# Performance work log

Hardware: AMD Instinct MI355X
Metric: run time of the kernel (lower is better)

Reference implementation:

```python
import jax, jax.numpy as jnp
import numpy as np

NEG_SLOPE = 0.2

def _spmm(row, col, val, emb, n_out):
    # sparse [n_out, n_src] @ emb[n_src, d] via gather + segment_sum
    msgs = val[:, None] * emb[col]  # [E, d]
    return jax.ops.segment_sum(msgs, row, num_segments=n_out)

def setup_inputs() -> dict:
    key = jax.random.key(0)
    ks = jax.random.split(key, 10)
    N_U, N_I, D = 100000, 200000, 64
    E_U, E_I = 1600000, 3200000
    return {
        "users_emb": jax.random.normal(ks[0], (N_U, D), dtype=jnp.float32),
        "items_emb": jax.random.normal(ks[1], (N_I, D), dtype=jnp.float32),
        "u_row": jax.random.randint(ks[2], (E_U,), 0, N_U, dtype=jnp.int32),
        "u_col": jax.random.randint(ks[3], (E_U,), 0, N_U, dtype=jnp.int32),
        "u_val": jax.random.uniform(ks[4], (E_U,), dtype=jnp.float32),
        "i_row": jax.random.randint(ks[5], (E_I,), 0, N_I, dtype=jnp.int32),
        "i_col": jax.random.randint(ks[6], (E_I,), 0, N_I, dtype=jnp.int32),
        "i_val": jax.random.uniform(ks[7], (E_I,), dtype=jnp.float32),
        "W_u": jax.random.normal(ks[8], (D, D), dtype=jnp.float32) * (6.0 / (D + D)) ** 0.5,
        "W_i": jax.random.normal(ks[9], (D, D), dtype=jnp.float32) * (6.0 / (D + D)) ** 0.5,
    }

def reference(users_emb, items_emb, u_row, u_col, u_val, i_row, i_col, i_val, W_u, W_i):
    h_u = _spmm(u_row, u_col, u_val, users_emb, users_emb.shape[0])
    h_u = jax.nn.leaky_relu(h_u @ W_u, negative_slope=NEG_SLOPE)
    h_i = _spmm(i_row, i_col, i_val, items_emb, items_emb.shape[0])
    h_i = jax.nn.leaky_relu(h_i @ W_i, negative_slope=NEG_SLOPE)
    return (h_u, h_i)
```

## Files before the change

kernel.cpp:

```cpp
#include <hip/hip_runtime.h>

#define NEG_SLOPE 0.2f

typedef unsigned int u32;

__device__ __forceinline__ unsigned short f32_to_bf16_rne(float f) {
    u32 u = __float_as_uint(f);
    u = (u + 0x7FFFu + ((u >> 16) & 1u)) >> 16;
    return (unsigned short)u;
}
__device__ __forceinline__ float bf16_to_f32(unsigned short b) {
    return __uint_as_float(((u32)b) << 16);
}

__global__ void spmm_scatter_kernel(const float* __restrict__ emb,
                                    const int* __restrict__ row,
                                    const int* __restrict__ col,
                                    const float* __restrict__ val,
                                    float* __restrict__ acc,
                                    int n_edges) {
    const int lane = threadIdx.x & 63;
    const int wpb = blockDim.x >> 6;
    const int wib = threadIdx.x >> 6;
    const int total_waves = gridDim.x * wpb;
    for (int e = blockIdx.x * wpb + wib; e < n_edges; e += total_waves) {
        const int r = row[e];
        const int c = col[e];
        const float v = val[e];
        atomicAdd(&acc[(size_t)r * 64 + lane], v * emb[(size_t)c * 64 + lane]);
    }
}

__global__ void transform_leaky_kernel(float* __restrict__ io,
                                       const float* __restrict__ W_u,
                                       const float* __restrict__ W_i,
                                       int n_u_rows, int n_total_rows) {
    __shared__ float Ws[2][64 * 64];
    for (int i = threadIdx.x; i < 64 * 64; i += blockDim.x) {
        Ws[0][i] = W_u[i];
        Ws[1][i] = W_i[i];
    }
    __syncthreads();
    const int lane = threadIdx.x & 63;
    const int wpb = blockDim.x >> 6;
    const int wib = threadIdx.x >> 6;
    const int total_waves = gridDim.x * wpb;
    for (int r = blockIdx.x * wpb + wib; r < n_total_rows; r += total_waves) {
        const float* W = (r < n_u_rows) ? Ws[0] : Ws[1];
        const float hv = io[(size_t)r * 64 + lane];
        float acc = 0.0f;
        #pragma unroll
        for (int k = 0; k < 64; ++k) {
            const float hk = __shfl(hv, k, 64);
            acc = fmaf(hk, W[k * 64 + lane], acc);
        }
        io[(size_t)r * 64 + lane] = acc > 0.0f ? acc : NEG_SLOPE * acc;
    }
}

#define PT_ROWS 64
__global__ void pretransform_both_kernel(const float* __restrict__ uemb,
                                         const float* __restrict__ iemb,
                                         const float* __restrict__ W_u,
                                         const float* __restrict__ W_i,
                                         unsigned short* __restrict__ Ybf,
                                         int n_u, int n_i, int tiles_u) {
    __shared__ float Ws[64 * 64];
    __shared__ float hs[PT_ROWS][68];

    const int tile = blockIdx.x;
    const bool is_u = tile < tiles_u;
    const float* __restrict__ emb = is_u ? uemb : iemb;
    const float* __restrict__ W = is_u ? W_u : W_i;
    const int lt = is_u ? tile : tile - tiles_u;
    const int nr = is_u ? n_u : n_i;
    const int base = lt * PT_ROWS;
    const int rows_here = min(PT_ROWS, nr - base);
    const size_t ybase = (is_u ? (size_t)base : (size_t)n_u + base) * 64;

    const int lane = threadIdx.x & 63;
    const int wid  = threadIdx.x >> 6;
    const int rsub = lane >> 4;
    const int jg   = lane & 15;

    {
        const float4* src = (const float4*)W;
        float4* dst = (float4*)Ws;
        for (int i = threadIdx.x; i < 64 * 16; i += blockDim.x) dst[i] = src[i];
    }
    for (int i = threadIdx.x; i < rows_here * 16; i += blockDim.x) {
        const int r = i >> 4, q = i & 15;
        const float4 v = ((const float4*)(emb + (size_t)(base + r) * 64))[q];
        *(float4*)&hs[r][q * 4] = v;
    }
    __syncthreads();

    #pragma unroll
    for (int quad = 0; quad < 4; ++quad) {
        const int r = (wid + quad * 4) * 4 + rsub;
        if (r < rows_here) {
            float ax = 0.f, ay = 0.f, az = 0.f, aw = 0.f;
            #pragma unroll
            for (int kq = 0; kq < 16; ++kq) {
                const float4 h = *(const float4*)&hs[r][kq * 4];
                const float4 w0 = *(const float4*)&Ws[(kq * 4 + 0) * 64 + jg * 4];
                const float4 w1 = *(const float4*)&Ws[(kq * 4 + 1) * 64 + jg * 4];
                const float4 w2 = *(const float4*)&Ws[(kq * 4 + 2) * 64 + jg * 4];
                const float4 w3 = *(const float4*)&Ws[(kq * 4 + 3) * 64 + jg * 4];
                ax = fmaf(h.x, w0.x, ax); ay = fmaf(h.x, w0.y, ay);
                az = fmaf(h.x, w0.z, az); aw = fmaf(h.x, w0.w, aw);
                ax = fmaf(h.y, w1.x, ax); ay = fmaf(h.y, w1.y, ay);
                az = fmaf(h.y, w1.z, az); aw = fmaf(h.y, w1.w, aw);
                ax = fmaf(h.z, w2.x, ax); ay = fmaf(h.z, w2.y, ay);
                az = fmaf(h.z, w2.z, az); aw = fmaf(h.z, w2.w, aw);
                ax = fmaf(h.w, w3.x, ax); ay = fmaf(h.w, w3.y, ay);
                az = fmaf(h.w, w3.z, az); aw = fmaf(h.w, w3.w, aw);
            }
            ushort4 o;
            o.x = f32_to_bf16_rne(ax);
            o.y = f32_to_bf16_rne(ay);
            o.z = f32_to_bf16_rne(az);
            o.w = f32_to_bf16_rne(aw);
            *(ushort4*)(Ybf + ybase + (size_t)r * 64 + jg * 4) = o;
        }
    }
}

__global__ void hist_fine_kernel(const int* __restrict__ rows, int n_edges,
                                 int row_off, int* __restrict__ counts, int nfb) {
    extern __shared__ int lh[];
    for (int i = threadIdx.x; i < nfb; i += blockDim.x) lh[i] = 0;
    __syncthreads();
    const int tid = blockIdx.x * blockDim.x + threadIdx.x;
    const int stride = gridDim.x * blockDim.x;
    const int n4 = n_edges >> 2;
    for (int g = tid; g < n4; g += stride) {
        const int4 r4 = ((const int4*)rows)[g];
        atomicAdd(&lh[(row_off + r4.x) >> 6], 1);
        atomicAdd(&lh[(row_off + r4.y) >> 6], 1);
        atomicAdd(&lh[(row_off + r4.z) >> 6], 1);
        atomicAdd(&lh[(row_off + r4.w) >> 6], 1);
    }
    for (int e = (n4 << 2) + tid; e < n_edges; e += stride)
        atomicAdd(&lh[(row_off + rows[e]) >> 6], 1);
    __syncthreads();
    for (int i = threadIdx.x; i < nfb; i += blockDim.x) {
        const int c = lh[i];
        if (c) atomicAdd(&counts[i], c);
    }
}

__global__ void pad_counts_kernel(const int* __restrict__ cnt,
                                  int* __restrict__ pcnt, int nfb) {
    const int i = blockIdx.x * blockDim.x + threadIdx.x;
    if (i < nfb) pcnt[i] = (cnt[i] + 7) & ~7;
}

__global__ void scan_part1_kernel(const int* __restrict__ counts, int n,
                                  int* __restrict__ partials) {
    __shared__ int s[512];
    const int gi = blockIdx.x * 512 + threadIdx.x;
    s[threadIdx.x] = (gi < n) ? counts[gi] : 0;
    __syncthreads();
    for (int off = 256; off > 0; off >>= 1) {
        if (threadIdx.x < off) s[threadIdx.x] += s[threadIdx.x + off];
        __syncthreads();
    }
    if (threadIdx.x == 0) partials[blockIdx.x] = s[0];
}

__global__ void scan_part2_kernel(int* __restrict__ partials, int nb) {
    __shared__ int s[1024];
    const int tid = threadIdx.x;
    int v = (tid < nb) ? partials[tid] : 0;
    s[tid] = v;
    __syncthreads();
    for (int off = 1; off < 1024; off <<= 1) {
        int t = (tid >= off) ? s[tid - off] : 0;
        __syncthreads();
        s[tid] += t;
        __syncthreads();
    }
    if (tid < nb) partials[tid] = s[tid] - v;
}

__global__ void scan_part3_kernel(const int* __restrict__ counts, int n,
                                  const int* __restrict__ partials,
                                  int* __restrict__ row_ptr) {
    __shared__ int s[512];
    const int tid = threadIdx.x;
    const int gi = blockIdx.x * 512 + tid;
    const int v = (gi < n) ? counts[gi] : 0;
    s[tid] = v;
    __syncthreads();
    for (int off = 1; off < 512; off <<= 1) {
        int t = (tid >= off) ? s[tid - off] : 0;
        __syncthreads();
        s[tid] += t;
        __syncthreads();
    }
    const int base = partials[blockIdx.x];
    if (gi < n) {
        row_ptr[gi] = base + s[tid] - v;
        if (gi == n - 1) row_ptr[n] = base + s[tid];
    }
}

#define FPC 128

__global__ void init_coarse_kernel(const int* __restrict__ cnt,
                                   const int* __restrict__ fstart,
                                   int* __restrict__ cstart,
                                   int* __restrict__ ccnt,
                                   int* __restrict__ gcurA,
                                   int nfb, int ncb) {
    const int t = threadIdx.x;
    if (t < ncb) {
        const int s = fstart[t * FPC];
        cstart[t] = s;
        gcurA[t] = s;
        int sum = 0;
        for (int j = 0; j < FPC; ++j) {
            const int idx = t * FPC + j;
            if (idx < nfb) sum += cnt[idx];
        }
        ccnt[t] = sum;
    }
    if (t == ncb) cstart[ncb] = fstart[nfb];
}

__global__ void copy_gfcur_kernel(const int* __restrict__ fstart,
                                  int* __restrict__ gfcur, int nfb) {
    const int i = blockIdx.x * blockDim.x + threadIdx.x;
    if (i < nfb) gfcur[i] = fstart[i];
}

#define TA 2048
__global__ void passA_kernel(const int* __restrict__ rows,
                             const int* __restrict__ cols,
                             const float* __restrict__ vals,
                             int n_edges, int row_off, int col_off,
                             int* __restrict__ gcurA,
                             int2* __restrict__ stagA, int ncb) {
    __shared__ int elo[TA], ehi[TA], ebk[TA];
    __shared__ int cnt[64], base[64], gb[64];
    const int tid = threadIdx.x;
    const int tstart = blockIdx.x * TA;
    const int tn = min(TA, n_edges - tstart);

    if (tid < 64) cnt[tid] = 0;
    __syncthreads();

    int mylo[8], myhi[8], mycb[8], myrk[8];
    #pragma unroll
    for (int j = 0; j < 8; ++j) {
        const int t = tid + j * 256;
        mycb[j] = -1;
        if (t < tn) {
            const int e = tstart + t;
            const int r = row_off + rows[e];
            const int c = col_off + cols[e];
            const int cb = r >> 13;
            mylo[j] = c | ((r & 8191) << 19);
            myhi[j] = __float_as_int(vals[e]);
            mycb[j] = cb;
            myrk[j] = atomicAdd(&cnt[cb], 1);
        }
    }
    __syncthreads();
    if (tid == 0) {
        int acc = 0;
        for (int b = 0; b < ncb; ++b) { base[b] = acc; acc += cnt[b]; }
    }
    if (tid < ncb) gb[tid] = atomicAdd(&gcurA[tid], cnt[tid]);
    __syncthreads();
    #pragma unroll
    for (int j = 0; j < 8; ++j) {
        if (mycb[j] >= 0) {
            const int pos = base[mycb[j]] + myrk[j];
            elo[pos] = mylo[j];
            ehi[pos] = myhi[j];
            ebk[pos] = mycb[j];
        }
    }
    __syncthreads();
    #pragma unroll
    for (int j = 0; j < 8; ++j) {
        const int t = tid + j * 256;
        if (t < tn) {
            const int b = ebk[t];
            stagA[gb[b] + (t - base[b])] = make_int2(elo[t], ehi[t]);
        }
    }
}

#define TB 2048
#define KB 64
__global__ void passB_kernel(const int2* __restrict__ stagA,
                             const int* __restrict__ cstart,
                             const int* __restrict__ ccnt,
                             int* __restrict__ gfcur,
                             int2* __restrict__ stagB, int nfb) {
    __shared__ int elo[TB], ehi[TB];
    __shared__ int cnt[FPC], base[FPC], gb[FPC];
    const int tid = threadIdx.x;
    const int cb = blockIdx.x / KB;
    const int k  = blockIdx.x % KB;
    const int s = cstart[cb];
    const int n = ccnt[cb];
    const int chunk = (n + KB - 1) / KB;
    const int lo_i = k * chunk;
    const int hi_i = min(n, lo_i + chunk);

    for (int t0 = lo_i; t0 < hi_i; t0 += TB) {
        const int tn = min(TB, hi_i - t0);

        __syncthreads();
        if (tid < FPC) cnt[tid] = 0;
        __syncthreads();

        int mylo[8], myhi[8], myfb[8], myrk[8];
        #pragma unroll
        for (int j = 0; j < 8; ++j) {
            const int t = tid + j * 256;
            myfb[j] = -1;
            if (t < tn) {
                const int2 e = stagA[s + t0 + t];
                const int f = (int)(((u32)e.x) >> 25);
                mylo[j] = e.x;
                myhi[j] = e.y;
                myfb[j] = f;
                myrk[j] = atomicAdd(&cnt[f], 1);
            }
        }
        __syncthreads();
        if (tid == 0) {
            int acc = 0;
            for (int b = 0; b < FPC; ++b) { base[b] = acc; acc += cnt[b]; }
        }
        if (tid < FPC) {
            const int idx = cb * FPC + tid;
            gb[tid] = (idx < nfb && cnt[tid] > 0) ? atomicAdd(&gfcur[idx], cnt[tid]) : 0;
        }
        __syncthreads();
        #pragma unroll
        for (int j = 0; j < 8; ++j) {
            if (myfb[j] >= 0) {
                const int pos = base[myfb[j]] + myrk[j];
                elo[pos] = mylo[j];
                ehi[pos] = myhi[j];
            }
        }
        __syncthreads();
        #pragma unroll
        for (int j = 0; j < 8; ++j) {
            const int t = tid + j * 256;
            if (t < tn) {
                const int b = (int)(((u32)elo[t]) >> 25);
                stagB[gb[b] + (t - base[b])] = make_int2(elo[t], ehi[t]);
            }
        }
    }
}

#define EC 2048
__global__ void passC_kernel(const unsigned short* __restrict__ Ybf,
                             const int2* __restrict__ stagB,
                             const int* __restrict__ fstart,
                             const int* __restrict__ cnt,
                             float* __restrict__ out, int n_rows) {
    __shared__ int2 eds[EC];
    __shared__ int rcnt[64];
    __shared__ int rptr[65];
    const int tid = threadIdx.x;
    const int lane = tid & 63;
    const int wid = tid >> 6;
    const int fb = blockIdx.x;
    const int s = fstart[fb];
    const int n = cnt[fb];
    const int row0 = fb << 6;
    const int rows_here = min(64, n_rows - row0);

    if (n == 0) {
        for (int i = tid; i < rows_here * 16; i += 256)
            ((float4*)(out + (size_t)row0 * 64))[i] = make_float4(0.f, 0.f, 0.f, 0.f);
        return;
    }

    if (tid < 64) rcnt[tid] = 0;
    __syncthreads();

    int mylo[8], myhi[8], myrb[8], myrk[8];
    #pragma unroll
    for (int j = 0; j < 8; ++j) {
        const int t = tid + j * 256;
        myrb[j] = -1;
        if (t < n && t < EC) {
            const int2 e = stagB[s + t];
            const int rb = (e.x >> 19) & 63;
            mylo[j] = e.x;
            myhi[j] = e.y;
            myrb[j] = rb;
            myrk[j] = atomicAdd(&rcnt[rb], 1);
        }
    }
    __syncthreads();
    if (tid == 0) {
        int acc = 0;
        for (int b = 0; b < 64; ++b) { rptr[b] = acc; acc += rcnt[b]; }
        rptr[64] = acc;
    }
    __syncthreads();

    for (int h = 0; h < 2; ++h) {
        const int hbase = rptr[h * 32];
        #pragma unroll
        for (int j = 0; j < 8; ++j) {
            const int rb = myrb[j];
            if (rb >= h * 32 && rb < (h + 1) * 32) {
                const int pos = rptr[rb] + myrk[j] - hbase;
                if (pos < EC) eds[pos] = make_int2(mylo[j], myhi[j]);
            }
        }
        __syncthreads();
        for (int rr = 0; rr < 8; ++rr) {
            const int rl = h * 32 + wid * 8 + rr;
            const int js = rptr[rl] - hbase;
            const int je = rptr[rl + 1] - hbase;
            float a0 = 0.f, a1 = 0.f, a2 = 0.f, a3 = 0.f;
            int j = js;
            for (; j + 4 <= je; j += 4) {
                const int2 e0 = eds[j];
                const int2 e1 = eds[j + 1];
                const int2 e2 = eds[j + 2];
                const int2 e3 = eds[j + 3];
                const float y0 = bf16_to_f32(Ybf[(size_t)(e0.x & 0x7FFFF) * 64 + lane]);
                const float y1 = bf16_to_f32(Ybf[(size_t)(e1.x & 0x7FFFF) * 64 + lane]);
                const float y2 = bf16_to_f32(Ybf[(size_t)(e2.x & 0x7FFFF) * 64 + lane]);
                const float y3 = bf16_to_f32(Ybf[(size_t)(e3.x & 0x7FFFF) * 64 + lane]);
                a0 = fmaf(__int_as_float(e0.y), y0, a0);
                a1 = fmaf(__int_as_float(e1.y), y1, a1);
                a2 = fmaf(__int_as_float(e2.y), y2, a2);
                a3 = fmaf(__int_as_float(e3.y), y3, a3);
            }
            for (; j < je; ++j) {
                const int2 e0 = eds[j];
                a0 = fmaf(__int_as_float(e0.y),
                          bf16_to_f32(Ybf[(size_t)(e0.x & 0x7FFFF) * 64 + lane]), a0);
            }
            const int rgl = row0 + rl;
            if (rgl < n_rows) {
                const float a = (a0 + a1) + (a2 + a3);
                out[(size_t)rgl * 64 + lane] = a > 0.f ? a : NEG_SLOPE * a;
            }
        }
        __syncthreads();
    }
}

extern "C" void kernel_launch(void* const* d_in, const int* in_sizes, int n_in,
                              void* d_out, int out_size, void* d_ws, size_t ws_size,
                              hipStream_t stream) {
    const float* users_emb = (const float*)d_in[0];
    const float* items_emb = (const float*)d_in[1];
    const int*   u_row     = (const int*)d_in[2];
    const int*   u_col     = (const int*)d_in[3];
    const float* u_val     = (const float*)d_in[4];
    const int*   i_row     = (const int*)d_in[5];
    const int*   i_col     = (const int*)d_in[6];
    const float* i_val     = (const float*)d_in[7];
    const float* W_u       = (const float*)d_in[8];
    const float* W_i       = (const float*)d_in[9];

    const int n_u = in_sizes[0] / 64;
    const int n_i = in_sizes[1] / 64;
    const int e_u = in_sizes[2];
    const int e_i = in_sizes[5];
    const int n_rows = n_u + n_i;
    const long long E = (long long)e_u + e_i;

    float* out = (float*)d_out;

    const int BLK = 256;
    const int nfb = (n_rows + 63) >> 6;
    const int ncb = (n_rows + 8191) >> 13;
    const int nb = (nfb + 511) / 512;
    const long long EPAD = E + (long long)nfb * 8;

    size_t off = 0;
    #define ALIGN4 off = (off + 3) & ~(size_t)3
    const size_t o_cnt    = off;  off += (size_t)nfb;        ALIGN4;
    const size_t o_pcnt   = off;  off += (size_t)nfb;        ALIGN4;
    const size_t o_fstart = off;  off += (size_t)nfb + 1;    ALIGN4;
    const size_t o_part   = off;  off += (size_t)nb;         ALIGN4;
    const size_t o_cstart = off;  off += (size_t)ncb + 1;    ALIGN4;
    const size_t o_ccnt   = off;  off += (size_t)ncb;        ALIGN4;
    const size_t o_gcurA  = off;  off += (size_t)ncb;        ALIGN4;
    const size_t o_gfcur  = off;  off += (size_t)nfb;        ALIGN4;
    const size_t o_Y      = off;  off += (size_t)n_rows * 32; ALIGN4;
    const size_t o_stagA  = off;  off += (size_t)EPAD * 2;   ALIGN4;
    const size_t o_stagB  = off;  off += (size_t)EPAD * 2;
    const size_t need_bytes = off * 4;

    if (ws_size >= need_bytes && nb <= 1024 && ncb <= 63) {
        int*            cnt    = (int*)d_ws + o_cnt;
        int*            pcnt   = (int*)d_ws + o_pcnt;
        int*            fstart = (int*)d_ws + o_fstart;
        int*            part   = (int*)d_ws + o_part;
        int*            cstart = (int*)d_ws + o_cstart;
        int*            ccnt   = (int*)d_ws + o_ccnt;
        int*            gcurA  = (int*)d_ws + o_gcurA;
        int*            gfcur  = (int*)d_ws + o_gfcur;
        unsigned short* Ybf    = (unsigned short*)((int*)d_ws + o_Y);
        int2*           stagA  = (int2*)((int*)d_ws + o_stagA);
        int2*           stagB  = (int2*)((int*)d_ws + o_stagB);

        const int tiles_u = (n_u + PT_ROWS - 1) / PT_ROWS;
        const int tiles_i = (n_i + PT_ROWS - 1) / PT_ROWS;
        pretransform_both_kernel<<<tiles_u + tiles_i, BLK, 0, stream>>>(
            users_emb, items_emb, W_u, W_i, Ybf, n_u, n_i, tiles_u);

        hipMemsetAsync(cnt, 0, (size_t)nfb * 4, stream);
        const size_t hist_lds = (size_t)nfb * 4;
        hist_fine_kernel<<<512, BLK, hist_lds, stream>>>(u_row, e_u, 0, cnt, nfb);
        hist_fine_kernel<<<512, BLK, hist_lds, stream>>>(i_row, e_i, n_u, cnt, nfb);

        pad_counts_kernel<<<(nfb + BLK - 1) / BLK, BLK, 0, stream>>>(cnt, pcnt, nfb);
        scan_part1_kernel<<<nb, 512, 0, stream>>>(pcnt, nfb, part);
        scan_part2_kernel<<<1, 1024, 0, stream>>>(part, nb);
        scan_part3_kernel<<<nb, 512, 0, stream>>>(pcnt, nfb, part, fstart);

        init_coarse_kernel<<<1, 64, 0, stream>>>(cnt, fstart, cstart, ccnt,
                                                 gcurA, nfb, ncb);
        copy_gfcur_kernel<<<(nfb + BLK - 1) / BLK, BLK, 0, stream>>>(fstart, gfcur, nfb);

        passA_kernel<<<(e_u + TA - 1) / TA, BLK, 0, stream>>>(
            u_row, u_col, u_val, e_u, 0, 0, gcurA, stagA, ncb);
        passA_kernel<<<(e_i + TA - 1) / TA, BLK, 0, stream>>>(
            i_row, i_col, i_val, e_i, n_u, n_u, gcurA, stagA, ncb);

        passB_kernel<<<ncb * KB, BLK, 0, stream>>>(stagA, cstart, ccnt,
                                                   gfcur, stagB, nfb);

        passC_kernel<<<nfb, BLK, 0, stream>>>(Ybf, stagB, fstart, cnt, out, n_rows);
    } else {
        float* out_u = out;
        float* out_i = out + (size_t)n_u * 64;
        hipMemsetAsync(d_out, 0, (size_t)out_size * sizeof(float), stream);
        const int WPB = BLK / 64;
        int grid_u = (e_u + WPB - 1) / WPB;
        int grid_i = (e_i + WPB - 1) / WPB;
        const int SCAP = 256 * 8;
        if (grid_u > SCAP) grid_u = SCAP;
        if (grid_i > SCAP) grid_i = SCAP;
        spmm_scatter_kernel<<<grid_u, BLK, 0, stream>>>(users_emb, u_row, u_col, u_val, out_u, e_u);
        spmm_scatter_kernel<<<grid_i, BLK, 0, stream>>>(items_emb, i_row, i_col, i_val, out_i, e_i);
        int grid_t = (n_rows + WPB - 1) / WPB;
        if (grid_t > 2048) grid_t = 2048;
        transform_leaky_kernel<<<grid_t, BLK, 0, stream>>>(out, W_u, W_i, n_u, n_rows);
    }
}
```

Measured before the change: 367.3 us.

## Merge histogram, scan, and pass-A launches into fewer fused kernels

Merges the two per-graph histogram kernels into one and the two passA launches into one grid that picks user or item edges by block index. The pad/scan/coarse-init/copy chain of six small kernels becomes a single 1024-thread scan_init kernel that also computes coarse counts in shared memory. The aim is to cut launch count and inter-kernel gaps in the preprocessing phase. Trade-offs are that the scan now runs serially on one block, the fast path is limited to nfb<=8192, and loc[8] caps items per thread at 8.

```diff
diff --git a/kernel.cpp b/kernel.cpp
--- a/kernel.cpp
+++ b/kernel.cpp
@@ -126,23 +126,37 @@
     }
 }
 
-__global__ void hist_fine_kernel(const int* __restrict__ rows, int n_edges,
-                                 int row_off, int* __restrict__ counts, int nfb) {
+__global__ void hist_fine2_kernel(const int* __restrict__ r1, int e1,
+                                  const int* __restrict__ r2, int e2,
+                                  int off2, int* __restrict__ counts, int nfb) {
     extern __shared__ int lh[];
     for (int i = threadIdx.x; i < nfb; i += blockDim.x) lh[i] = 0;
     __syncthreads();
     const int tid = blockIdx.x * blockDim.x + threadIdx.x;
     const int stride = gridDim.x * blockDim.x;
-    const int n4 = n_edges >> 2;
-    for (int g = tid; g < n4; g += stride) {
-        const int4 r4 = ((const int4*)rows)[g];
-        atomicAdd(&lh[(row_off + r4.x) >> 6], 1);
-        atomicAdd(&lh[(row_off + r4.y) >> 6], 1);
-        atomicAdd(&lh[(row_off + r4.z) >> 6], 1);
-        atomicAdd(&lh[(row_off + r4.w) >> 6], 1);
-    }
-    for (int e = (n4 << 2) + tid; e < n_edges; e += stride)
-        atomicAdd(&lh[(row_off + rows[e]) >> 6], 1);
+
+    const int n41 = e1 >> 2;
+    for (int g = tid; g < n41; g += stride) {
+        const int4 r4 = ((const int4*)r1)[g];
+        atomicAdd(&lh[r4.x >> 6], 1);
+        atomicAdd(&lh[r4.y >> 6], 1);
+        atomicAdd(&lh[r4.z >> 6], 1);
+        atomicAdd(&lh[r4.w >> 6], 1);
+    }
+    for (int e = (n41 << 2) + tid; e < e1; e += stride)
+        atomicAdd(&lh[r1[e] >> 6], 1);
+
+    const int n42 = e2 >> 2;
+    for (int g = tid; g < n42; g += stride) {
+        const int4 r4 = ((const int4*)r2)[g];
+        atomicAdd(&lh[(off2 + r4.x) >> 6], 1);
+        atomicAdd(&lh[(off2 + r4.y) >> 6], 1);
+        atomicAdd(&lh[(off2 + r4.z) >> 6], 1);
+        atomicAdd(&lh[(off2 + r4.w) >> 6], 1);
+    }
+    for (int e = (n42 << 2) + tid; e < e2; e += stride)
+        atomicAdd(&lh[(off2 + r2[e]) >> 6], 1);
+
     __syncthreads();
     for (int i = threadIdx.x; i < nfb; i += blockDim.x) {
         const int c = lh[i];
@@ -150,30 +164,39 @@
     }
 }
 
-__global__ void pad_counts_kernel(const int* __restrict__ cnt,
-                                  int* __restrict__ pcnt, int nfb) {
-    const int i = blockIdx.x * blockDim.x + threadIdx.x;
-    if (i < nfb) pcnt[i] = (cnt[i] + 7) & ~7;
-}
-
-__global__ void scan_part1_kernel(const int* __restrict__ counts, int n,
-                                  int* __restrict__ partials) {
-    __shared__ int s[512];
-    const int gi = blockIdx.x * 512 + threadIdx.x;
-    s[threadIdx.x] = (gi < n) ? counts[gi] : 0;
-    __syncthreads();
-    for (int off = 256; off > 0; off >>= 1) {
-        if (threadIdx.x < off) s[threadIdx.x] += s[threadIdx.x + off];
-        __syncthreads();
-    }
-    if (threadIdx.x == 0) partials[blockIdx.x] = s[0];
-}
-
-__global__ void scan_part2_kernel(int* __restrict__ partials, int nb) {
-    __shared__ int s[1024];
+#define FPC 128
+
+__global__ void scan_init_kernel(const int* __restrict__ cnt, int nfb, int ncb,
+                                 int* __restrict__ fstart,
+                                 int* __restrict__ gfcur,
+                                 int* __restrict__ cstart,
+                                 int* __restrict__ ccnt,
+                                 int* __restrict__ gcurA) {
+    extern __shared__ int smem[];
+    int* s   = smem;
+    int* sfs = smem + 1024;
+    int* sc  = smem + 1024 + nfb + 1;
+
     const int tid = threadIdx.x;
-    int v = (tid < nb) ? partials[tid] : 0;
-    s[tid] = v;
+    const int ipt = (nfb + 1023) >> 10;
+    if (tid < 64) sc[tid] = 0;
+    __syncthreads();
+
+    int loc[8];
+    int sum = 0;
+    const int b0 = tid * ipt;
+    for (int k = 0; k < ipt; ++k) {
+        const int i = b0 + k;
+        int v = 0;
+        if (i < nfb) {
+            const int c = cnt[i];
+            v = (c + 7) & ~7;
+            atomicAdd(&sc[i >> 7], c);
+        }
+        loc[k] = sum;
+        sum += v;
+    }
+    s[tid] = sum;
     __syncthreads();
     for (int off = 1; off < 1024; off <<= 1) {
         int t = (tid >= off) ? s[tid - off] : 0;
@@ -181,71 +204,54 @@
         s[tid] += t;
         __syncthreads();
     }
-    if (tid < nb) partials[tid] = s[tid] - v;
-}
-
-__global__ void scan_part3_kernel(const int* __restrict__ counts, int n,
-                                  const int* __restrict__ partials,
-                                  int* __restrict__ row_ptr) {
-    __shared__ int s[512];
-    const int tid = threadIdx.x;
-    const int gi = blockIdx.x * 512 + tid;
-    const int v = (gi < n) ? counts[gi] : 0;
-    s[tid] = v;
-    __syncthreads();
-    for (int off = 1; off < 512; off <<= 1) {
-        int t = (tid >= off) ? s[tid - off] : 0;
-        __syncthreads();
-        s[tid] += t;
-        __syncthreads();
-    }
-    const int base = partials[blockIdx.x];
-    if (gi < n) {
-        row_ptr[gi] = base + s[tid] - v;
-        if (gi == n - 1) row_ptr[n] = base + s[tid];
-    }
-}
-
-#define FPC 128
-
-__global__ void init_coarse_kernel(const int* __restrict__ cnt,
-                                   const int* __restrict__ fstart,
-                                   int* __restrict__ cstart,
-                                   int* __restrict__ ccnt,
-                                   int* __restrict__ gcurA,
-                                   int nfb, int ncb) {
-    const int t = threadIdx.x;
-    if (t < ncb) {
-        const int s = fstart[t * FPC];
-        cstart[t] = s;
-        gcurA[t] = s;
-        int sum = 0;
-        for (int j = 0; j < FPC; ++j) {
-            const int idx = t * FPC + j;
-            if (idx < nfb) sum += cnt[idx];
-        }
-        ccnt[t] = sum;
-    }
-    if (t == ncb) cstart[ncb] = fstart[nfb];
-}
-
-__global__ void copy_gfcur_kernel(const int* __restrict__ fstart,
-                                  int* __restrict__ gfcur, int nfb) {
-    const int i = blockIdx.x * blockDim.x + threadIdx.x;
-    if (i < nfb) gfcur[i] = fstart[i];
+    const int excl = s[tid] - sum;
+    for (int k = 0; k < ipt; ++k) {
+        const int i = b0 + k;
+        if (i < nfb) {
+            const int f = excl + loc[k];
+            fstart[i] = f;
+            gfcur[i] = f;
+            sfs[i] = f;
+        }
+    }
+    if (tid == 0) {
+        const int tot = s[1023];
+        fstart[nfb] = tot;
+        sfs[nfb] = tot;
+    }
+    __syncthreads();
+
+    if (tid < ncb) {
+        const int st = sfs[min(tid * FPC, nfb)];
+        cstart[tid] = st;
+        gcurA[tid] = st;
+        ccnt[tid] = sc[tid];
+    }
+    if (tid == ncb) cstart[ncb] = sfs[nfb];
 }
 
 #define TA 2048
-__global__ void passA_kernel(const int* __restrict__ rows,
-                             const int* __restrict__ cols,
-                             const float* __restrict__ vals,
-                             int n_edges, int row_off, int col_off,
-                             int* __restrict__ gcurA,
-                             int2* __restrict__ stagA, int ncb) {
+__global__ void passA2_kernel(const int* __restrict__ u_row,
+                              const int* __restrict__ u_col,
+                              const float* __restrict__ u_val, int e_u,
+                              const int* __restrict__ i_row,
+                              const int* __restrict__ i_col,
+                              const float* __restrict__ i_val, int e_i,
+                              int n_u, int tiles_u,
+                              int* __restrict__ gcurA,
+                              int2* __restrict__ stagA, int ncb) {
     __shared__ int elo[TA], ehi[TA], ebk[TA];
     __shared__ int cnt[64], base[64], gb[64];
     const int tid = threadIdx.x;
-    const int tstart = blockIdx.x * TA;
+    const int bid = blockIdx.x;
+
+    const bool is_u = bid < tiles_u;
+    const int* __restrict__ rows = is_u ? u_row : i_row;
+    const int* __restrict__ cols = is_u ? u_col : i_col;
+    const float* __restrict__ vals = is_u ? u_val : i_val;
+    const int n_edges = is_u ? e_u : e_i;
+    const int off = is_u ? 0 : n_u;
+    const int tstart = (is_u ? bid : bid - tiles_u) * TA;
     const int tn = min(TA, n_edges - tstart);
 
     if (tid < 64) cnt[tid] = 0;
@@ -258,8 +264,8 @@
         mycb[j] = -1;
         if (t < tn) {
             const int e = tstart + t;
-            const int r = row_off + rows[e];
-            const int c = col_off + cols[e];
+            const int r = off + rows[e];
+            const int c = off + cols[e];
             const int cb = r >> 13;
             mylo[j] = c | ((r & 8191) << 19);
             myhi[j] = __float_as_int(vals[e]);
@@ -272,7 +278,7 @@
         int acc = 0;
         for (int b = 0; b < ncb; ++b) { base[b] = acc; acc += cnt[b]; }
     }
-    if (tid < ncb) gb[tid] = atomicAdd(&gcurA[tid], cnt[tid]);
+    if (tid < ncb) gb[tid] = (cnt[tid] > 0) ? atomicAdd(&gcurA[tid], cnt[tid]) : 0;
     __syncthreads();
     #pragma unroll
     for (int j = 0; j < 8; ++j) {
@@ -380,6 +386,7 @@
     const int n = cnt[fb];
     const int row0 = fb << 6;
     const int rows_here = min(64, n_rows - row0);
+    const unsigned short* __restrict__ Yl = Ybf + lane;
 
     if (n == 0) {
         for (int i = tid; i < rows_here * 16; i += 256)
@@ -434,10 +441,10 @@
                 const int2 e1 = eds[j + 1];
                 const int2 e2 = eds[j + 2];
                 const int2 e3 = eds[j + 3];
-                const float y0 = bf16_to_f32(Ybf[(size_t)(e0.x & 0x7FFFF) * 64 + lane]);
-                const float y1 = bf16_to_f32(Ybf[(size_t)(e1.x & 0x7FFFF) * 64 + lane]);
-                const float y2 = bf16_to_f32(Ybf[(size_t)(e2.x & 0x7FFFF) * 64 + lane]);
-                const float y3 = bf16_to_f32(Ybf[(size_t)(e3.x & 0x7FFFF) * 64 + lane]);
+                const float y0 = bf16_to_f32(Yl[(size_t)(e0.x & 0x7FFFF) * 64]);
+                const float y1 = bf16_to_f32(Yl[(size_t)(e1.x & 0x7FFFF) * 64]);
+                const float y2 = bf16_to_f32(Yl[(size_t)(e2.x & 0x7FFFF) * 64]);
+                const float y3 = bf16_to_f32(Yl[(size_t)(e3.x & 0x7FFFF) * 64]);
                 a0 = fmaf(__int_as_float(e0.y), y0, a0);
                 a1 = fmaf(__int_as_float(e1.y), y1, a1);
                 a2 = fmaf(__int_as_float(e2.y), y2, a2);
@@ -446,7 +453,7 @@
             for (; j < je; ++j) {
                 const int2 e0 = eds[j];
                 a0 = fmaf(__int_as_float(e0.y),
-                          bf16_to_f32(Ybf[(size_t)(e0.x & 0x7FFFF) * 64 + lane]), a0);
+                          bf16_to_f32(Yl[(size_t)(e0.x & 0x7FFFF) * 64]), a0);
             }
             const int rgl = row0 + rl;
             if (rgl < n_rows) {
@@ -484,15 +491,12 @@
     const int BLK = 256;
     const int nfb = (n_rows + 63) >> 6;
     const int ncb = (n_rows + 8191) >> 13;
-    const int nb = (nfb + 511) / 512;
     const long long EPAD = E + (long long)nfb * 8;
 
     size_t off = 0;
     #define ALIGN4 off = (off + 3) & ~(size_t)3
     const size_t o_cnt    = off;  off += (size_t)nfb;        ALIGN4;
-    const size_t o_pcnt   = off;  off += (size_t)nfb;        ALIGN4;
     const size_t o_fstart = off;  off += (size_t)nfb + 1;    ALIGN4;
-    const size_t o_part   = off;  off += (size_t)nb;         ALIGN4;
     const size_t o_cstart = off;  off += (size_t)ncb + 1;    ALIGN4;
     const size_t o_ccnt   = off;  off += (size_t)ncb;        ALIGN4;
     const size_t o_gcurA  = off;  off += (size_t)ncb;        ALIGN4;
@@ -502,11 +506,9 @@
     const size_t o_stagB  = off;  off += (size_t)EPAD * 2;
     const size_t need_bytes = off * 4;
 
-    if (ws_size >= need_bytes && nb <= 1024 && ncb <= 63) {
+    if (ws_size >= need_bytes && nfb <= 8192 && ncb <= 63) {
         int*            cnt    = (int*)d_ws + o_cnt;
-        int*            pcnt   = (int*)d_ws + o_pcnt;
         int*            fstart = (int*)d_ws + o_fstart;
-        int*            part   = (int*)d_ws + o_part;
         int*            cstart = (int*)d_ws + o_cstart;
         int*            ccnt   = (int*)d_ws + o_ccnt;
         int*            gcurA  = (int*)d_ws + o_gcurA;
@@ -515,29 +517,25 @@
         int2*           stagA  = (int2*)((int*)d_ws + o_stagA);
         int2*           stagB  = (int2*)((int*)d_ws + o_stagB);
 
-        const int tiles_u = (n_u + PT_ROWS - 1) / PT_ROWS;
-        const int tiles_i = (n_i + PT_ROWS - 1) / PT_ROWS;
-        pretransform_both_kernel<<<tiles_u + tiles_i, BLK, 0, stream>>>(
-            users_emb, items_emb, W_u, W_i, Ybf, n_u, n_i, tiles_u);
+        const int tiles_u_pt = (n_u + PT_ROWS - 1) / PT_ROWS;
+        const int tiles_i_pt = (n_i + PT_ROWS - 1) / PT_ROWS;
+        pretransform_both_kernel<<<tiles_u_pt + tiles_i_pt, BLK, 0, stream>>>(
+            users_emb, items_emb, W_u, W_i, Ybf, n_u, n_i, tiles_u_pt);
 
         hipMemsetAsync(cnt, 0, (size_t)nfb * 4, stream);
         const size_t hist_lds = (size_t)nfb * 4;
-        hist_fine_kernel<<<512, BLK, hist_lds, stream>>>(u_row, e_u, 0, cnt, nfb);
-        hist_fine_kernel<<<512, BLK, hist_lds, stream>>>(i_row, e_i, n_u, cnt, nfb);
-
-        pad_counts_kernel<<<(nfb + BLK - 1) / BLK, BLK, 0, stream>>>(cnt, pcnt, nfb);
-        scan_part1_kernel<<<nb, 512, 0, stream>>>(pcnt, nfb, part);
-        scan_part2_kernel<<<1, 1024, 0, stream>>>(part, nb);
-        scan_part3_kernel<<<nb, 512, 0, stream>>>(pcnt, nfb, part, fstart);
-
-        init_coarse_kernel<<<1, 64, 0, stream>>>(cnt, fstart, cstart, ccnt,
-                                                 gcurA, nfb, ncb);
-        copy_gfcur_kernel<<<(nfb + BLK - 1) / BLK, BLK, 0, stream>>>(fstart, gfcur, nfb);
-
-        passA_kernel<<<(e_u + TA - 1) / TA, BLK, 0, stream>>>(
-            u_row, u_col, u_val, e_u, 0, 0, gcurA, stagA, ncb);
-        passA_kernel<<<(e_i + TA - 1) / TA, BLK, 0, stream>>>(
-            i_row, i_col, i_val, e_i, n_u, n_u, gcurA, stagA, ncb);
+        hist_fine2_kernel<<<512, BLK, hist_lds, stream>>>(u_row, e_u, i_row, e_i,
+                                                          n_u, cnt, nfb);
+
+        const size_t si_lds = (size_t)(1024 + nfb + 1 + 64) * 4;
+        scan_init_kernel<<<1, 1024, si_lds, stream>>>(cnt, nfb, ncb, fstart,
+                                                      gfcur, cstart, ccnt, gcurA);
+
+        const int tiles_u_a = (e_u + TA - 1) / TA;
+        const int tiles_i_a = (e_i + TA - 1) / TA;
+        passA2_kernel<<<tiles_u_a + tiles_i_a, BLK, 0, stream>>>(
+            u_row, u_col, u_val, e_u, i_row, i_col, i_val, e_i,
+            n_u, tiles_u_a, gcurA, stagA, ncb);
 
         passB_kernel<<<ncb * KB, BLK, 0, stream>>>(stagA, cstart, ccnt,
                                                    gfcur, stagB, nfb);
```

After: 340.0 us. 1.08x faster.
